# Kernel optimization log

Hardware: AMD Instinct MI355X
Metric: run time of the kernel (lower is better)

The kernel has to match this reference:

```python
import jax, jax.numpy as jnp
import numpy as np

N = 100000          # num nodes
E = 500000          # num edges
D_IN = 32           # in_channels
D_OUT = 32          # out_channels (== in_channels, required by per-edge bmm)
NUM_REL = 16


def setup_inputs() -> dict:
    key = jax.random.key(0)
    k1, k2, k3, k4, k5, k6 = jax.random.split(key, 6)
    x = jax.random.normal(k1, (N, D_IN), dtype=jnp.float32)
    edge_index = jax.random.randint(k2, (2, E), 0, N)
    edge_type = jax.random.randint(k3, (E,), 0, NUM_REL)
    # Linear(in, out, bias=False): weight stored [in, out] here (x @ W)
    W = jax.random.normal(k4, (D_IN, D_OUT), dtype=jnp.float32) / np.sqrt(D_IN)
    # nn.Embedding(num_relations, in*out)
    rel_emb = jax.random.normal(k5, (NUM_REL, D_IN * D_OUT), dtype=jnp.float32)
    # attention vector, xavier-uniform-ish
    lim = float(1.414 * np.sqrt(6.0 / (D_OUT + 1)))
    attention = jax.random.uniform(k6, (D_OUT, 1), minval=-lim, maxval=lim, dtype=jnp.float32)
    return {"x": x, "edge_index": edge_index, "edge_type": edge_type,
            "W": W, "rel_emb": rel_emb, "attention": attention}


def reference(x, edge_index, edge_type, W, rel_emb, attention):
    # x = self.weight(x)
    h = x @ W                                            # [N, D_OUT]
    # per-edge relation transform: rel_trans [E, D_IN, D_OUT]
    rel = rel_emb[edge_type].reshape(-1, D_IN, D_OUT)    # [E, D_IN, D_OUT]
    src = edge_index[0]
    dst = edge_index[1]
    # messages = bmm(x[src], rel_trans) -> per-edge matvec
    msg = jnp.einsum('ei,eio->eo', h[src], rel)          # [E, D_OUT]
    # scatter-add into destination node buckets
    out = jax.ops.segment_sum(msg, dst, num_segments=N)  # [N, D_OUT]
    # global attention softmax over all nodes (dim=0)
    scores = (out @ attention)[:, 0]                     # [N]
    weights = jax.nn.softmax(scores, axis=0)             # [N]
    # dropout omitted (eval mode / deterministic reference)
    out = jax.nn.relu(out * weights[:, None])
    return out
```

## Files before the change

### kernel.cpp

```cpp
#include <hip/hip_runtime.h>
#include <hip/hip_fp16.h>

static constexpr int NN  = 100000;
static constexpr int NE  = 500000;
static constexpr int D   = 32;
static constexpr int NR  = 16;
static constexpr int HB  = 256;
static constexpr int ES  = (NE + HB - 1) / HB;
static constexpr int CAP = 33000;
static constexpr int NY  = 128;

__global__ __launch_bounds__(256) void k_prep(const int* __restrict__ ei,
                                              const int* __restrict__ et,
                                              const float* __restrict__ W,
                                              const float* __restrict__ rel,
                                              float* __restrict__ wr,
                                              int* __restrict__ cursor,
                                              int2* __restrict__ rec,
                                              float4* __restrict__ zbase) {
    __shared__ int lh[NR], lcur[NR];
    if (threadIdx.x < NR) lh[threadIdx.x] = 0;
    __syncthreads();

    {
        const int total4 = (NN * D * 2 + NN * 4) / 16;
        for (int i = blockIdx.x * 256 + threadIdx.x; i < total4; i += HB * 256)
            zbase[i] = make_float4(0.f, 0.f, 0.f, 0.f);
    }

    if (blockIdx.x < NR) {
        const int t = blockIdx.x;
        for (int idx = threadIdx.x; idx < D * D; idx += 256) {
            const int i = idx >> 5;
            const int o = idx & 31;
            const float* Wr = W + i * D;
            const float* Rr = rel + t * (D * D) + o;
            float s = 0.f;
            #pragma unroll
            for (int j = 0; j < D; ++j)
                s = fmaf(Wr[j], Rr[j * D], s);
            wr[t * (D * D) + idx] = s;
        }
    }

    const int beg = blockIdx.x * ES, end = min(beg + ES, NE);
    for (int e = beg + (int)threadIdx.x; e < end; e += 256)
        atomicAdd(&lh[et[e]], 1);
    __syncthreads();
    if (threadIdx.x < NR)
        lcur[threadIdx.x] = (lh[threadIdx.x] > 0)
                          ? atomicAdd(&cursor[threadIdx.x], lh[threadIdx.x])
                          : 0;
    __syncthreads();
    for (int e = beg + (int)threadIdx.x; e < end; e += 256) {
        const int t = et[e];
        const int rank = min(atomicAdd(&lcur[t], 1), CAP - 1);
        rec[t * CAP + rank] = make_int2(ei[e], ei[NE + e]);
    }
}

__global__ __launch_bounds__(256) void k_edge(const float* __restrict__ x,
                                              const int2* __restrict__ rec,
                                              const int* __restrict__ cnt,
                                              const float* __restrict__ wr,
                                              const float* __restrict__ att,
                                              __half* __restrict__ acc16,
                                              float* __restrict__ scores) {
    const int t    = blockIdx.x & (NR - 1);
    const int c    = blockIdx.x >> 4;
    const int lane = threadIdx.x & 63;
    const int wv   = threadIdx.x >> 6;
    const int half = lane >> 5;
    const int o    = lane & 31;
    const int r8   = lane >> 3;
    const int q8   = lane & 7;

    __shared__ float sx[4][2][8][36];
    __shared__ int   sd[4][2][8];

    const float atto = att[o];
    float Rc[32];
    {
        const float* __restrict__ Rt = wr + t * 1024;
        #pragma unroll
        for (int i = 0; i < 32; ++i) Rc[i] = Rt[i * 32 + o];
    }

    const int beg  = t * CAP;
    const int cntt = min(cnt[t], CAP);
    if (cntt <= 0) return;
    const int elast = beg + cntt - 1;
    const int ngrp  = (cntt + 7) >> 3;
    const int nw    = NY * 4;
    const int wid   = c * 4 + wv;
    if (wid >= ngrp) return;

    int2 rr0 = rec[min(beg + wid * 8 + r8, elast)];
    int2 rr1 = rec[min(beg + (wid + nw) * 8 + r8, elast)];
    int2 rr2 = rec[min(beg + (wid + 2 * nw) * 8 + r8, elast)];
    float4 xv0 = reinterpret_cast<const float4*>(x + (size_t)rr0.x * D)[q8];

    int buf = 0;
    for (int grp = wid; grp < ngrp; grp += nw) {
        *reinterpret_cast<float4*>(&sx[wv][buf][r8][q8 * 4]) = xv0;
        if (q8 == 0) sd[wv][buf][r8] = rr0.y;

        float4 xv1 = reinterpret_cast<const float4*>(x + (size_t)rr1.x * D)[q8];
        int2 rr3 = rec[min(beg + (grp + 3 * nw) * 8 + r8, elast)];

        __asm__ volatile("s_waitcnt lgkmcnt(0)" ::: "memory");

        const int lbase = grp * 8;
        #pragma unroll
        for (int jj = 0; jj < 4; ++jj) {
            const int row = jj * 2 + half;
            const float* rp = &sx[wv][buf][row][0];
            float p = 0.f;
            #pragma unroll
            for (int q = 0; q < 8; ++q) {
                const float4 v = *reinterpret_cast<const float4*>(rp + q * 4);
                p = fmaf(v.x, Rc[4*q+0], p);
                p = fmaf(v.y, Rc[4*q+1], p);
                p = fmaf(v.z, Rc[4*q+2], p);
                p = fmaf(v.w, Rc[4*q+3], p);
            }
            if (lbase + row < cntt) {
                const int dd = sd[wv][buf][row];
                float v = p * atto;
                v += __shfl_xor(v, 1, 64);
                v += __shfl_xor(v, 2, 64);
                v += __shfl_xor(v, 4, 64);
                v += __shfl_xor(v, 8, 64);
                v += __shfl_xor(v, 16, 64);
                if (o == 0) atomicAdd(scores + dd, v);
                const float pp = __shfl_xor(p, 1, 64);
                if ((o & 1) == 0) {
                    __half2 hv = __halves2half2(__float2half(p), __float2half(pp));
                    unsafeAtomicAdd(reinterpret_cast<__half2*>(
                        acc16 + (size_t)dd * D + o), hv);
                }
            }
        }
        rr0 = rr1; rr1 = rr2; rr2 = rr3; xv0 = xv1;
        buf ^= 1;
    }
}

__global__ __launch_bounds__(256) void k_score(const float* __restrict__ scores,
                                               float* __restrict__ pmax,
                                               float* __restrict__ psum) {
    __shared__ float shm[4], shs[4];
    const int n = blockIdx.x * 256 + threadIdx.x;
    const float s = (n < NN) ? scores[n] : -3.4e38f;
    float m = s;
    #pragma unroll
    for (int offt = 32; offt > 0; offt >>= 1)
        m = fmaxf(m, __shfl_down(m, offt, 64));
    if ((threadIdx.x & 63) == 0) shm[threadIdx.x >> 6] = m;
    __syncthreads();
    const float bm = fmaxf(fmaxf(shm[0], shm[1]), fmaxf(shm[2], shm[3]));
    float e = (n < NN) ? expf(s - bm) : 0.f;
    #pragma unroll
    for (int offt = 32; offt > 0; offt >>= 1)
        e += __shfl_down(e, offt, 64);
    if ((threadIdx.x & 63) == 0) shs[threadIdx.x >> 6] = e;
    __syncthreads();
    if (threadIdx.x == 0) {
        pmax[blockIdx.x] = bm;
        psum[blockIdx.x] = shs[0] + shs[1] + shs[2] + shs[3];
    }
}

__global__ __launch_bounds__(256) void k_final(const __half* __restrict__ acc16,
                                               const float* __restrict__ scores,
                                               const float* __restrict__ pmax,
                                               const float* __restrict__ psum,
                                               float* __restrict__ out,
                                               int nb) {
    __shared__ float shm[4], shs[4];
    const int tid = threadIdx.x;
    float m = -3.4e38f, s = 0.f;
    for (int i = tid; i < nb; i += 256) {
        const float mi = pmax[i], si = psum[i];
        const float M = fmaxf(m, mi);
        s = s * expf(m - M) + si * expf(mi - M);
        m = M;
    }
    #pragma unroll
    for (int offt = 32; offt > 0; offt >>= 1) {
        const float mo = __shfl_down(m, offt, 64);
        const float so = __shfl_down(s, offt, 64);
        const float M = fmaxf(m, mo);
        s = s * expf(m - M) + so * expf(mo - M);
        m = M;
    }
    if ((tid & 63) == 0) { shm[tid >> 6] = m; shs[tid >> 6] = s; }
    __syncthreads();
    float M = shm[0], S = shs[0];
    #pragma unroll
    for (int w = 1; w < 4; ++w) {
        const float Mn = fmaxf(M, shm[w]);
        S = S * expf(M - Mn) + shs[w] * expf(shm[w] - Mn);
        M = Mn;
    }
    const int idx = blockIdx.x * 256 + tid;
    if (idx >= NN * 4) return;
    const int n  = idx >> 2;
    const int co = (idx & 3) * 8;
    const float w = expf(scores[n] - M) / S;
    const __half2* hp = reinterpret_cast<const __half2*>(acc16 + (size_t)n * D + co);
    float4 o0, o1;
    {
        float2 f0 = __half22float2(hp[0]);
        float2 f1 = __half22float2(hp[1]);
        float2 f2 = __half22float2(hp[2]);
        float2 f3 = __half22float2(hp[3]);
        o0.x = fmaxf(f0.x * w, 0.f); o0.y = fmaxf(f0.y * w, 0.f);
        o0.z = fmaxf(f1.x * w, 0.f); o0.w = fmaxf(f1.y * w, 0.f);
        o1.x = fmaxf(f2.x * w, 0.f); o1.y = fmaxf(f2.y * w, 0.f);
        o1.z = fmaxf(f3.x * w, 0.f); o1.w = fmaxf(f3.y * w, 0.f);
    }
    float4* op = reinterpret_cast<float4*>(out + (size_t)n * D + co);
    op[0] = o0;
    op[1] = o1;
}

extern "C" void kernel_launch(void* const* d_in, const int* in_sizes, int n_in,
                              void* d_out, int out_size, void* d_ws, size_t ws_size,
                              hipStream_t stream) {
    const float* x   = (const float*)d_in[0];
    const int*   ei  = (const int*)  d_in[1];
    const int*   et  = (const int*)  d_in[2];
    const float* W   = (const float*)d_in[3];
    const float* rel = (const float*)d_in[4];
    const float* att = (const float*)d_in[5];
    float* out = (float*)d_out;

    float*  wr     = (float*)d_ws;
    __half* acc16  = (__half*)(wr + NR * D * D);
    float*  scores = (float*)(acc16 + (size_t)NN * D);
    int2*   rec    = (int2*)(scores + NN);
    int*    cursor = (int*)(rec + NR * CAP);
    float*  pmax   = (float*)(cursor + NR);
    float*  psum   = pmax + 512;

    hipMemsetAsync(cursor, 0, NR * sizeof(int), stream);

    k_prep<<<HB, 256, 0, stream>>>(ei, et, W, rel, wr, cursor, rec,
                                   (float4*)acc16);
    k_edge<<<NR * NY, 256, 0, stream>>>(x, rec, cursor, wr, att, acc16, scores);

    const int nb_n = (NN + 255) / 256;
    k_score<<<nb_n, 256, 0, stream>>>(scores, pmax, psum);
    k_final<<<(NN * 4 + 255) / 256, 256, 0, stream>>>(acc16, scores, pmax, psum,
                                                      out, nb_n);
}
```

Baseline: 88.47 us.

## Use MFMA fp16 for per-edge transform and fold attention into precomputed vector

```diff
diff --git a/kernel.cpp b/kernel.cpp
--- a/kernel.cpp
+++ b/kernel.cpp
@@ -1,5 +1,8 @@
 #include <hip/hip_runtime.h>
 #include <hip/hip_fp16.h>
+
+typedef _Float16 f16x8 __attribute__((ext_vector_type(8)));
+typedef float    f32x4 __attribute__((ext_vector_type(4)));
 
 static constexpr int NN  = 100000;
 static constexpr int NE  = 500000;
@@ -14,10 +17,13 @@
                                               const int* __restrict__ et,
                                               const float* __restrict__ W,
                                               const float* __restrict__ rel,
-                                              float* __restrict__ wr,
+                                              const float* __restrict__ att,
+                                              _Float16* __restrict__ wrB,
+                                              float* __restrict__ v_att,
                                               int* __restrict__ cursor,
                                               int2* __restrict__ rec,
                                               float4* __restrict__ zbase) {
+    __shared__ float sWR[D * D];
     __shared__ int lh[NR], lcur[NR];
     if (threadIdx.x < NR) lh[threadIdx.x] = 0;
     __syncthreads();
@@ -39,7 +45,26 @@
             #pragma unroll
             for (int j = 0; j < D; ++j)
                 s = fmaf(Wr[j], Rr[j * D], s);
-            wr[t * (D * D) + idx] = s;
+            sWR[idx] = s;
+        }
+        __syncthreads();
+        if (threadIdx.x < D) {
+            float v = 0.f;
+            #pragma unroll
+            for (int o = 0; o < D; ++o)
+                v = fmaf(sWR[threadIdx.x * D + o], att[o], v);
+            v_att[t * D + threadIdx.x] = v;
+        }
+        if (threadIdx.x < 128) {
+            const int f  = threadIdx.x >> 6;
+            const int s  = threadIdx.x & 63;
+            const int cc = s & 15;
+            const int kc = s >> 4;
+            f16x8 hb;
+            #pragma unroll
+            for (int j = 0; j < 8; ++j)
+                hb[j] = (_Float16)sWR[(kc * 8 + j) * D + f * 16 + cc];
+            *reinterpret_cast<f16x8*>(wrB + ((size_t)(t * 2 + f) * 64 + s) * 8) = hb;
         }
     }
 
@@ -62,87 +87,78 @@
 __global__ __launch_bounds__(256) void k_edge(const float* __restrict__ x,
                                               const int2* __restrict__ rec,
                                               const int* __restrict__ cnt,
-                                              const float* __restrict__ wr,
-                                              const float* __restrict__ att,
+                                              const _Float16* __restrict__ wrB,
+                                              const float* __restrict__ v_att,
                                               __half* __restrict__ acc16,
                                               float* __restrict__ scores) {
     const int t    = blockIdx.x & (NR - 1);
     const int c    = blockIdx.x >> 4;
     const int lane = threadIdx.x & 63;
     const int wv   = threadIdx.x >> 6;
-    const int half = lane >> 5;
-    const int o    = lane & 31;
-    const int r8   = lane >> 3;
-    const int q8   = lane & 7;
-
-    __shared__ float sx[4][2][8][36];
-    __shared__ int   sd[4][2][8];
-
-    const float atto = att[o];
-    float Rc[32];
+    const int col  = lane & 15;
+    const int kc   = lane >> 4;
+
+    const f16x8 b0 = *reinterpret_cast<const f16x8*>(
+        wrB + ((size_t)(t * 2 + 0) * 64 + lane) * 8);
+    const f16x8 b1 = *reinterpret_cast<const f16x8*>(
+        wrB + ((size_t)(t * 2 + 1) * 64 + lane) * 8);
+    float vf[8];
     {
-        const float* __restrict__ Rt = wr + t * 1024;
+        const float* vp = v_att + t * D + kc * 8;
         #pragma unroll
-        for (int i = 0; i < 32; ++i) Rc[i] = Rt[i * 32 + o];
+        for (int j = 0; j < 8; ++j) vf[j] = vp[j];
     }
 
     const int beg  = t * CAP;
     const int cntt = min(cnt[t], CAP);
     if (cntt <= 0) return;
-    const int elast = beg + cntt - 1;
-    const int ngrp  = (cntt + 7) >> 3;
+    const int bend  = beg + cntt;
+    const int elast = bend - 1;
+    const int ntile = (cntt + 15) >> 4;
     const int nw    = NY * 4;
     const int wid   = c * 4 + wv;
-    if (wid >= ngrp) return;
-
-    int2 rr0 = rec[min(beg + wid * 8 + r8, elast)];
-    int2 rr1 = rec[min(beg + (wid + nw) * 8 + r8, elast)];
-    int2 rr2 = rec[min(beg + (wid + 2 * nw) * 8 + r8, elast)];
-    float4 xv0 = reinterpret_cast<const float4*>(x + (size_t)rr0.x * D)[q8];
-
-    int buf = 0;
-    for (int grp = wid; grp < ngrp; grp += nw) {
-        *reinterpret_cast<float4*>(&sx[wv][buf][r8][q8 * 4]) = xv0;
-        if (q8 == 0) sd[wv][buf][r8] = rr0.y;
-
-        float4 xv1 = reinterpret_cast<const float4*>(x + (size_t)rr1.x * D)[q8];
-        int2 rr3 = rec[min(beg + (grp + 3 * nw) * 8 + r8, elast)];
-
-        __asm__ volatile("s_waitcnt lgkmcnt(0)" ::: "memory");
-
-        const int lbase = grp * 8;
+
+    for (int tile = wid; tile < ntile; tile += nw) {
+        const int tbase = beg + tile * 16;
+        const int2 rr = rec[min(tbase + col, elast)];
+        const float4* xp = reinterpret_cast<const float4*>(
+            x + (size_t)rr.x * D + kc * 8);
+        const float4 xa = xp[0], xb = xp[1];
+
+        float sp = xa.x*vf[0] + xa.y*vf[1] + xa.z*vf[2] + xa.w*vf[3]
+                 + xb.x*vf[4] + xb.y*vf[5] + xb.z*vf[6] + xb.w*vf[7];
+        sp += __shfl_xor(sp, 16, 64);
+        sp += __shfl_xor(sp, 32, 64);
+        if (lane < 16 && tbase + lane < bend)
+            atomicAdd(scores + rr.y, sp);
+
+        f16x8 a;
+        a[0] = (_Float16)xa.x; a[1] = (_Float16)xa.y;
+        a[2] = (_Float16)xa.z; a[3] = (_Float16)xa.w;
+        a[4] = (_Float16)xb.x; a[5] = (_Float16)xb.y;
+        a[6] = (_Float16)xb.z; a[7] = (_Float16)xb.w;
+
+        const f32x4 z = {0.f, 0.f, 0.f, 0.f};
+        f32x4 c0 = __builtin_amdgcn_mfma_f32_16x16x32_f16(a, b0, z, 0, 0, 0);
+        f32x4 c1 = __builtin_amdgcn_mfma_f32_16x16x32_f16(a, b1, z, 0, 0, 0);
+
+        const int rbase = kc * 4;
         #pragma unroll
-        for (int jj = 0; jj < 4; ++jj) {
-            const int row = jj * 2 + half;
-            const float* rp = &sx[wv][buf][row][0];
-            float p = 0.f;
-            #pragma unroll
-            for (int q = 0; q < 8; ++q) {
-                const float4 v = *reinterpret_cast<const float4*>(rp + q * 4);
-                p = fmaf(v.x, Rc[4*q+0], p);
-                p = fmaf(v.y, Rc[4*q+1], p);
-                p = fmaf(v.z, Rc[4*q+2], p);
-                p = fmaf(v.w, Rc[4*q+3], p);
+        for (int j = 0; j < 4; ++j) {
+            const int rj  = rbase + j;
+            const int ddj = __shfl(rr.y, rj, 64);
+            const float p0 = c0[j], p1 = c1[j];
+            const float q0 = __shfl_xor(p0, 1, 64);
+            const float q1 = __shfl_xor(p1, 1, 64);
+            if ((tbase + rj < bend) && !(lane & 1)) {
+                __half2 h0 = __halves2half2(__float2half(p0), __float2half(q0));
+                __half2 h1 = __halves2half2(__float2half(p1), __float2half(q1));
+                unsafeAtomicAdd(reinterpret_cast<__half2*>(
+                    acc16 + (size_t)ddj * D + col), h0);
+                unsafeAtomicAdd(reinterpret_cast<__half2*>(
+                    acc16 + (size_t)ddj * D + 16 + col), h1);
             }
-            if (lbase + row < cntt) {
-                const int dd = sd[wv][buf][row];
-                float v = p * atto;
-                v += __shfl_xor(v, 1, 64);
-                v += __shfl_xor(v, 2, 64);
-                v += __shfl_xor(v, 4, 64);
-                v += __shfl_xor(v, 8, 64);
-                v += __shfl_xor(v, 16, 64);
-                if (o == 0) atomicAdd(scores + dd, v);
-                const float pp = __shfl_xor(p, 1, 64);
-                if ((o & 1) == 0) {
-                    __half2 hv = __halves2half2(__float2half(p), __float2half(pp));
-                    unsafeAtomicAdd(reinterpret_cast<__half2*>(
-                        acc16 + (size_t)dd * D + o), hv);
-                }
-            }
-        }
-        rr0 = rr1; rr1 = rr2; rr2 = rr3; xv0 = xv1;
-        buf ^= 1;
+        }
     }
 }
 
@@ -236,19 +252,21 @@
     const float* att = (const float*)d_in[5];
     float* out = (float*)d_out;
 
-    float*  wr     = (float*)d_ws;
-    __half* acc16  = (__half*)(wr + NR * D * D);
-    float*  scores = (float*)(acc16 + (size_t)NN * D);
-    int2*   rec    = (int2*)(scores + NN);
-    int*    cursor = (int*)(rec + NR * CAP);
-    float*  pmax   = (float*)(cursor + NR);
-    float*  psum   = pmax + 512;
+    _Float16* wrB   = (_Float16*)d_ws;
+    float*   v_att  = (float*)(wrB + (size_t)NR * 2 * 64 * 8);
+    __half*  acc16  = (__half*)(v_att + NR * D);
+    float*   scores = (float*)(acc16 + (size_t)NN * D);
+    int2*    rec    = (int2*)(scores + NN);
+    int*     cursor = (int*)(rec + NR * CAP);
+    float*   pmax   = (float*)(cursor + NR);
+    float*   psum   = pmax + 512;
 
     hipMemsetAsync(cursor, 0, NR * sizeof(int), stream);
 
-    k_prep<<<HB, 256, 0, stream>>>(ei, et, W, rel, wr, cursor, rec,
-                                   (float4*)acc16);
-    k_edge<<<NR * NY, 256, 0, stream>>>(x, rec, cursor, wr, att, acc16, scores);
+    k_prep<<<HB, 256, 0, stream>>>(ei, et, W, rel, att, wrB, v_att,
+                                   cursor, rec, (float4*)acc16);
+    k_edge<<<NR * NY, 256, 0, stream>>>(x, rec, cursor, wrB, v_att,
+                                        acc16, scores);
 
     const int nb_n = (NN + 255) / 256;
     k_score<<<nb_n, 256, 0, stream>>>(scores, pmax, psum);
```

Measured after the change: 110.7 us. +25.1%, slower.
